# Performance work log

Measured on AMD Instinct MI355X. Metric: run time of the kernel, lower is better.

## Reference

```python
import jax, jax.numpy as jnp
import numpy as np
import math

DEC = (4, 4, 4)  # (vertical=Y, horizontal=X, depth=Z)


def _idct_mat(N, dtype=jnp.float32):
    # orthonormal DCT-II matrix D[k,n]; IDCT (DCT-III ortho) is D.T
    k = jnp.arange(N, dtype=dtype)[:, None]
    n = jnp.arange(N, dtype=dtype)[None, :]
    D = jnp.cos(jnp.pi * (n + 0.5) * k / N)
    s = jnp.where(k == 0, jnp.sqrt(1.0 / N), jnp.sqrt(2.0 / N))
    return (s * D).T  # [n, k]: y[n] = sum_k IDCT[n,k] X[k]


def _permute_idct_coefs(x, dec):
    decY, decX, decZ = dec
    coefs = x.reshape(-1, decY * decX * decZ)
    chY, chX, chZ = (decY + 1) // 2, (decX + 1) // 2, (decZ + 1) // 2
    fhY, fhX, fhZ = decY // 2, decX // 2, decZ // 2
    sizes = [(chY, chX, chZ), (chY, chX, fhZ), (chY, fhX, chZ), (chY, fhX, fhZ),
             (fhY, chX, chZ), (fhY, chX, fhZ), (fhY, fhX, chZ), (fhY, fhX, fhZ)]
    nB = coefs.shape[0]
    value = jnp.zeros((nB, decY, decX, decZ), dtype=x.dtype)
    slices = [(slice(0, None, 2), slice(0, None, 2), slice(0, None, 2)),
              (slice(0, None, 2), slice(0, None, 2), slice(1, None, 2)),
              (slice(0, None, 2), slice(1, None, 2), slice(0, None, 2)),
              (slice(0, None, 2), slice(1, None, 2), slice(1, None, 2)),
              (slice(1, None, 2), slice(0, None, 2), slice(0, None, 2)),
              (slice(1, None, 2), slice(0, None, 2), slice(1, None, 2)),
              (slice(1, None, 2), slice(1, None, 2), slice(0, None, 2)),
              (slice(1, None, 2), slice(1, None, 2), slice(1, None, 2))]
    start = 0
    for (sy, sx, sz), (ny, nx, nz) in zip(slices, sizes):
        n = ny * nx * nz
        chunk = coefs[:, start:start + n].reshape(nB, ny, nx, nz)
        value = value.at[:, sy, sx, sz].set(chunk)
        start += n
    return value


def setup_inputs() -> dict:
    key = jax.random.key(0)
    x0 = jax.random.normal(key, (4, 64, 64, 64, DEC[0] * DEC[1] * DEC[2]), dtype=jnp.float32)
    return {"x0": x0}


def reference(x0) -> jnp.ndarray:
    nsamples, nrows, ncols, nlays, _ = x0.shape
    decY, decX, decZ = DEC
    V = _permute_idct_coefs(x0, DEC)  # [nBlocks, decY, decX, decZ]
    IY, IX, IZ = _idct_mat(decY, x0.dtype), _idct_mat(decX, x0.dtype), _idct_mat(decZ, x0.dtype)
    # separable 3D IDCT (orthonormal) along the three block axes
    Y = jnp.einsum('byxz,iy,jx,kz->bijk', V, IY, IX, IZ)
    height, width, depth = nrows * decY, ncols * decX, nlays * decZ
    Z = Y.reshape(nsamples, 1, height, width, depth)
    return Z
```

## Files before the change

kernel.cpp:

```cpp
#include <hip/hip_runtime.h>


#define WG 256
#define C1F 0.6532814824381883f
#define C3F 0.2705980500730985f

#define IDCT4(a0, a2, a1, a3, r0, r1, r2, r3)            \
    {                                                    \
        const float e0 = 0.5f * ((a0) + (a2));           \
        const float e1 = 0.5f * ((a0) - (a2));           \
        const float o0 = C1F * (a1) + C3F * (a3);        \
        const float o1 = C3F * (a1) - C1F * (a3);        \
        (r0) = e0 + o0;                                  \
        (r1) = e1 + o1;                                  \
        (r2) = e1 - o1;                                  \
        (r3) = e0 - o0;                                  \
    }

__global__ __launch_bounds__(WG) void nsolt_idct3d_kernel(
    const float* __restrict__ in, float* __restrict__ out)
{
    __shared__ float lds[64 * 64];
    const int t = threadIdx.x;
    const int w = t >> 6;
    const int l = t & 63;
    const size_t wgbase = (size_t)blockIdx.x * 4096;

    {
        const int c   = l & 15;
        const int rlo = l >> 4;
#pragma unroll
        for (int m = 0; m < 4; ++m) {
            const int r = w * 16 + m * 4 + rlo;
            const int h = (r << 4) | (c ^ rlo ^ (4 * (m & 1)));
            const float* src = in + wgbase + (size_t)h * 4;
            __builtin_amdgcn_global_load_lds(
                (const __attribute__((address_space(1))) void*)src,
                (__attribute__((address_space(3))) void*)(&lds[(w * 256 + m * 64) * 4]),
                16, 0, 0);
        }
    }
    __syncthreads();

    const int gW = t >> 2;
    const int j  = t & 3;
    const int c1 = j & 1;
    const int c2 = j >> 1;
    const int s7 = gW & 7;
    float* __restrict__ myblk = &lds[gW * 64];

    float qa[16];
#pragma unroll
    for (int k = 0; k < 4; ++k) {
        const float4 v = *reinterpret_cast<const float4*>(
            &myblk[(((4 * j + k) ^ s7) << 2)]);
        qa[k * 4 + 0] = v.x; qa[k * 4 + 1] = v.y;
        qa[k * 4 + 2] = v.z; qa[k * 4 + 3] = v.w;
    }

    float A[2][2][4];
#pragma unroll
    for (int w2 = 0; w2 < 2; ++w2) {
#pragma unroll
        for (int w1 = 0; w1 < 2; ++w1) {
            const float a0 = qa[w2 * 4 + 2 * w1];
            const float a2 = qa[w2 * 4 + 2 * w1 + 1];
            const float a1 = qa[(2 + w2) * 4 + 2 * w1];
            const float a3 = qa[(2 + w2) * 4 + 2 * w1 + 1];
            IDCT4(a0, a2, a1, a3,
                  A[w2][w1][0], A[w2][w1][1], A[w2][w1][2], A[w2][w1][3]);
        }
    }

    const float xk0 = c1 ? C3F : 0.5f;
    const float xk1 = c1 ? -C1F : 0.5f;
    const float xs0 = c1 ? C1F : 0.5f;
    const float xs1 = c1 ? C3F : -0.5f;
    const float xsg = c1 ? -1.0f : 1.0f;

    float X[2][2][4];
#pragma unroll
    for (int w2 = 0; w2 < 2; ++w2) {
#pragma unroll
        for (int n = 0; n < 4; ++n) {
            const float A0 = A[w2][0][n], A1 = A[w2][1][n];
            const float uk = xk0 * A0 + xk1 * A1;
            const float us = xs0 * A0 + xs1 * A1;
            const float rv = __shfl_xor(us, 1, 64);
            X[w2][0][n] = uk + rv;
            X[w2][1][n] = xsg * (uk - rv);
        }
    }

    const float yk0 = c2 ? C3F : 0.5f;
    const float yk1 = c2 ? -C1F : 0.5f;
    const float ys0 = c2 ? C1F : 0.5f;
    const float ys1 = c2 ? C3F : -0.5f;
    const float ysg = c2 ? -1.0f : 1.0f;

    const int xa = c1 ? 1 : 0, xb = c1 ? 2 : 3;
    const int ya = c2 ? 1 : 0, yb = c2 ? 2 : 3;

#pragma unroll
    for (int xs = 0; xs < 2; ++xs) {
        float ra[4], rb[4];
#pragma unroll
        for (int n = 0; n < 4; ++n) {
            const float A0 = X[0][xs][n], A1 = X[1][xs][n];
            const float uk = yk0 * A0 + yk1 * A1;
            const float us = ys0 * A0 + ys1 * A1;
            const float rv = __shfl_xor(us, 2, 64);
            ra[n] = uk + rv;
            rb[n] = ysg * (uk - rv);
        }
        const int xv = xs ? xb : xa;
        float4 va; va.x = ra[0]; va.y = ra[1]; va.z = ra[2]; va.w = ra[3];
        float4 vb; vb.x = rb[0]; vb.y = rb[1]; vb.z = rb[2]; vb.w = rb[3];
        *reinterpret_cast<float4*>(&myblk[(((ya * 4 + xv) ^ s7) << 2)]) = va;
        *reinterpret_cast<float4*>(&myblk[(((yb * 4 + xv) ^ s7) << 2)]) = vb;
    }
    __syncthreads();

    {
        const int c   = l & 15;
        const int rlo = l >> 4;
#pragma unroll
        for (int m = 0; m < 4; ++m) {
            const int f = w * 256 + m * 64 + l;
            const float4 v = *reinterpret_cast<const float4*>(&lds[f * 4]);
            const int r = w * 16 + m * 4 + rlo;
            const int h = (r << 4) | (c ^ rlo ^ (4 * (m & 1)));
            *reinterpret_cast<float4*>(out + wgbase + (size_t)h * 4) = v;
        }
    }
}

extern "C" void kernel_launch(void* const* d_in, const int* in_sizes, int n_in,
                              void* d_out, int out_size, void* d_ws, size_t ws_size,
                              hipStream_t stream)
{
    const float* in = (const float*)d_in[0];
    float* out = (float*)d_out;

    const long long nBlocks = (long long)in_sizes[0] / 64;
    const int grid = (int)(nBlocks / 64);

    hipLaunchKernelGGL(nsolt_idct3d_kernel, dim3(grid), dim3(WG), 0, stream,
                       in, out);
}
```

Measured before the change: 99.96 us.

## Make each wavefront loop over tiles with register double-buffered prefetch

Each wavefront now owns a private 16-block LDS region and processes eight consecutive tiles in a persistent loop. Two tiles are prefetched into registers so the global loads for later tiles overlap the current tile's LDS transpose and IDCT. Workgroup barriers are removed in favour of wave-local LDS use. Output goes through nontemporal stores. The direct global-to-LDS loads are replaced by register loads plus LDS stores, and the grid shrinks eightfold, which may reduce the number of loads in flight.

```diff
diff --git a/kernel.cpp b/kernel.cpp
--- a/kernel.cpp
+++ b/kernel.cpp
@@ -2,8 +2,11 @@
 
 
 #define WG 256
+#define NT 8
 #define C1F 0.6532814824381883f
 #define C3F 0.2705980500730985f
+
+typedef float vfloat4 __attribute__((ext_vector_type(4)));
 
 #define IDCT4(a0, a2, a1, a3, r0, r1, r2, r3)            \
     {                                                    \
@@ -17,42 +20,46 @@
         (r3) = e0 - o0;                                  \
     }
 
-__global__ __launch_bounds__(WG) void nsolt_idct3d_kernel(
-    const float* __restrict__ in, float* __restrict__ out)
+__device__ __forceinline__ int swz(int c) {
+    return (c & ~15) | ((c & 15) ^ ((c >> 4) & 7));
+}
+
+__device__ __forceinline__ void load_tile(vfloat4 s[4],
+                                          const float* __restrict__ in,
+                                          size_t tb, int l) {
+#pragma unroll
+    for (int m = 0; m < 4; ++m)
+        s[m] = *reinterpret_cast<const vfloat4*>(in + tb + m * 256 + l * 4);
+}
+
+__device__ __forceinline__ void process_tile(
+    vfloat4 s[4], bool doPrefetch, size_t nextTb,
+    const float* __restrict__ in, float* __restrict__ out,
+    size_t tb, float* __restrict__ region, int l)
 {
-    __shared__ float lds[64 * 64];
-    const int t = threadIdx.x;
-    const int w = t >> 6;
-    const int l = t & 63;
-    const size_t wgbase = (size_t)blockIdx.x * 4096;
+#pragma unroll
+    for (int m = 0; m < 4; ++m) {
+        const int c = m * 64 + l;
+        *reinterpret_cast<vfloat4*>(&region[swz(c) * 4]) = s[m];
+    }
 
-    {
-        const int c   = l & 15;
-        const int rlo = l >> 4;
+    if (doPrefetch) {
 #pragma unroll
-        for (int m = 0; m < 4; ++m) {
-            const int r = w * 16 + m * 4 + rlo;
-            const int h = (r << 4) | (c ^ rlo ^ (4 * (m & 1)));
-            const float* src = in + wgbase + (size_t)h * 4;
-            __builtin_amdgcn_global_load_lds(
-                (const __attribute__((address_space(1))) void*)src,
-                (__attribute__((address_space(3))) void*)(&lds[(w * 256 + m * 64) * 4]),
-                16, 0, 0);
-        }
+        for (int m = 0; m < 4; ++m)
+            s[m] = *reinterpret_cast<const vfloat4*>(in + nextTb + m * 256 + l * 4);
     }
-    __syncthreads();
 
-    const int gW = t >> 2;
-    const int j  = t & 3;
+    const int gW = l >> 2;
+    const int j  = l & 3;
     const int c1 = j & 1;
     const int c2 = j >> 1;
     const int s7 = gW & 7;
-    float* __restrict__ myblk = &lds[gW * 64];
+    float* __restrict__ myblk = &region[gW * 64];
 
     float qa[16];
 #pragma unroll
     for (int k = 0; k < 4; ++k) {
-        const float4 v = *reinterpret_cast<const float4*>(
+        const vfloat4 v = *reinterpret_cast<const vfloat4*>(
             &myblk[(((4 * j + k) ^ s7) << 2)]);
         qa[k * 4 + 0] = v.x; qa[k * 4 + 1] = v.y;
         qa[k * 4 + 2] = v.z; qa[k * 4 + 3] = v.w;
@@ -114,24 +121,41 @@
             rb[n] = ysg * (uk - rv);
         }
         const int xv = xs ? xb : xa;
-        float4 va; va.x = ra[0]; va.y = ra[1]; va.z = ra[2]; va.w = ra[3];
-        float4 vb; vb.x = rb[0]; vb.y = rb[1]; vb.z = rb[2]; vb.w = rb[3];
-        *reinterpret_cast<float4*>(&myblk[(((ya * 4 + xv) ^ s7) << 2)]) = va;
-        *reinterpret_cast<float4*>(&myblk[(((yb * 4 + xv) ^ s7) << 2)]) = vb;
+        vfloat4 va; va.x = ra[0]; va.y = ra[1]; va.z = ra[2]; va.w = ra[3];
+        vfloat4 vb; vb.x = rb[0]; vb.y = rb[1]; vb.z = rb[2]; vb.w = rb[3];
+        *reinterpret_cast<vfloat4*>(&myblk[(((ya * 4 + xv) ^ s7) << 2)]) = va;
+        *reinterpret_cast<vfloat4*>(&myblk[(((yb * 4 + xv) ^ s7) << 2)]) = vb;
     }
-    __syncthreads();
 
-    {
-        const int c   = l & 15;
-        const int rlo = l >> 4;
 #pragma unroll
-        for (int m = 0; m < 4; ++m) {
-            const int f = w * 256 + m * 64 + l;
-            const float4 v = *reinterpret_cast<const float4*>(&lds[f * 4]);
-            const int r = w * 16 + m * 4 + rlo;
-            const int h = (r << 4) | (c ^ rlo ^ (4 * (m & 1)));
-            *reinterpret_cast<float4*>(out + wgbase + (size_t)h * 4) = v;
-        }
+    for (int m = 0; m < 4; ++m) {
+        const int f = m * 64 + l;
+        const vfloat4 v = *reinterpret_cast<const vfloat4*>(&region[f * 4]);
+        __builtin_nontemporal_store(
+            v, reinterpret_cast<vfloat4*>(out + tb + (size_t)swz(f) * 4));
+    }
+}
+
+__global__ __launch_bounds__(WG, 2) void nsolt_idct3d_kernel(
+    const float* __restrict__ in, float* __restrict__ out)
+{
+    __shared__ float lds[4 * 1024];
+    const int t = threadIdx.x;
+    const int l = t & 63;
+    const int wv = blockIdx.x * (WG / 64) + (t >> 6);
+    float* __restrict__ region = &lds[(t >> 6) * 1024];
+
+    const size_t tile0 = (size_t)wv * NT;
+
+    vfloat4 sA[4], sB[4];
+    load_tile(sA, in, tile0 * 1024, l);
+    load_tile(sB, in, (tile0 + 1) * 1024, l);
+
+    for (int it = 0; it < NT; it += 2) {
+        process_tile(sA, it + 2 < NT, (tile0 + it + 2) * 1024,
+                     in, out, (tile0 + it) * 1024, region, l);
+        process_tile(sB, it + 3 < NT, (tile0 + it + 3) * 1024,
+                     in, out, (tile0 + it + 1) * 1024, region, l);
     }
 }
 
@@ -142,8 +166,9 @@
     const float* in = (const float*)d_in[0];
     float* out = (float*)d_out;
 
-    const long long nBlocks = (long long)in_sizes[0] / 64;
-    const int grid = (int)(nBlocks / 64);
+    const long long nfloat = (long long)in_sizes[0];
+    const long long nTiles = nfloat / 1024;
+    const int grid = (int)(nTiles / (NT * (WG / 64)));
 
     hipLaunchKernelGGL(nsolt_idct3d_kernel, dim3(grid), dim3(WG), 0, stream,
                        in, out);
```

Result: faster. 83.21 us (-16.8%).
